# Kernel tuning notes

Hardware: AMD Instinct MI355X
Metric: run time of the kernel (lower is better)

Reference implementation:

```python
import jax, jax.numpy as jnp
import numpy as np

B, S, D = 64, 256, 768   # batch, max_seq_length, bert hidden
CAP = 8                  # semantic_cap_size (= num_capsules)
NT = 10                  # ntasks (= num_routes)
TASK = 5
NUM_ITER = 3


def squash(t, axis=-1):
    sq = jnp.sum(t * t, axis=axis, keepdims=True)
    return (sq / (1.0 + sq)) * t / jnp.sqrt(sq)


def setup_inputs() -> dict:
    key = jax.random.key(0)
    k0, k1, k2, k3 = jax.random.split(key, 4)
    x = jax.random.normal(k0, (B, S, D), dtype=jnp.float32)
    # per-task semantic projections: ntasks x Linear(768 -> CAP)
    fc1_w = jax.random.normal(k1, (NT, CAP, D), dtype=jnp.float32) * 0.02
    fc1_b = jnp.zeros((NT, CAP), dtype=jnp.float32)
    # route_weights: [num_capsules, num_routes, in_channel=S*CAP, class_dim=S]
    route_weights = jax.random.normal(k2, (CAP, NT, S * CAP, S), dtype=jnp.float32)
    # larger: Linear(CAP -> 768)
    larger_w = jax.random.normal(k3, (D, CAP), dtype=jnp.float32) * 0.02
    larger_b = jnp.zeros((D,), dtype=jnp.float32)
    return {"x": x, "task": TASK, "fc1_w": fc1_w, "fc1_b": fc1_b,
            "route_weights": route_weights, "larger_w": larger_w, "larger_b": larger_b}


def reference(x, task, fc1_w, fc1_b, route_weights, larger_w, larger_b):
    Bb, Ss, _ = x.shape
    nt, cap, _ = fc1_w.shape
    # --- semantic capsules: per-task Linear, cat over task dim, squash over tasks ---
    sem = jnp.einsum('bsd,ncd->bscn', x, fc1_w) + fc1_b.T[None, None]  # [B,S,CAP,NT]
    sem = sem.reshape(Bb, Ss * cap, nt)          # matches torch view(B,-1,1)+cat
    sem = squash(sem, axis=-1)
    u = jnp.transpose(sem, (0, 2, 1))            # [B, NT, S*CAP] (transpose(2,1))
    # --- tsv capsules: dynamic routing ---
    priors = jnp.einsum('brk,crkl->cbrl', u, route_weights)[:, :, :, None, :]  # [CAP,B,NT,1,S]
    tsv = jnp.tril(jnp.ones((nt, nt), dtype=x.dtype))
    tsv_t = tsv[task].reshape(1, 1, nt, 1, 1)
    mask = jnp.where(tsv[task] == 0, jnp.float32(-10000.0), jnp.float32(0.0)).reshape(1, 1, nt, 1, 1)
    logits = jnp.zeros_like(priors)
    vote = None
    for i in range(NUM_ITER):
        logits = logits * tsv_t + mask
        probs = jax.nn.softmax(logits, axis=2)                     # softmax over routes
        vote = jnp.sum(probs * priors, axis=2, keepdims=True)      # [CAP,B,1,1,S]
        out = squash(vote, axis=-1)
        if i != NUM_ITER - 1:
            logits = logits + jnp.sum(priors * out, axis=-1, keepdims=True)
    # torch .view on contiguous [CAP,B,1,1,S] -> (B, S, CAP): row-major reinterpret
    h = vote.reshape(-1).reshape(Bb, Ss, cap)
    return h @ larger_w.T + larger_b
```

## Files before the change

### kernel.cpp

```cpp
#include <hip/hip_runtime.h>
#include <hip/hip_bf16.h>

#define Bq 64
#define Sq 256
#define Dq 768
#define CAPq 8
#define NTq 10
#define SCq 2048

typedef short bf16x8 __attribute__((ext_vector_type(8)));
typedef float f32x4  __attribute__((ext_vector_type(4)));

static __device__ __forceinline__ short bfhi(float f) {
    return (short)(__float_as_uint(f) >> 16);
}
static __device__ __forceinline__ short bflo(float f) {
    float hi = __uint_as_float(__float_as_uint(f) & 0xFFFF0000u);
    return (short)(__float_as_uint(f - hi) >> 16);
}

__global__ __launch_bounds__(256) void k0_cvt(const float* __restrict__ w,
                                              short* __restrict__ hi,
                                              short* __restrict__ lo) {
    int i = blockIdx.x * 256 + threadIdx.x;
    if (i < NTq * CAPq * Dq) {
        int k8 = i / 640;
        int rem = i - k8 * 640;
        int o = rem >> 3, kf = rem & 7;
        float f = w[o * Dq + k8 * 8 + kf];
        hi[i] = bfhi(f);
        lo[i] = bflo(f);
    }
}

__device__ __forceinline__ void k1_comp(const float* xv, const short* pwh, const short* pwl,
                                        int ko80, f32x4* acc) {
    bf16x8 ah, al;
#pragma unroll
    for (int i = 0; i < 8; ++i) { ah[i] = bfhi(xv[i]); al[i] = bflo(xv[i]); }
#pragma unroll
    for (int f = 0; f < 5; ++f) {
        bf16x8 bh = *reinterpret_cast<const bf16x8*>(pwh + ko80 + f * 128);
        bf16x8 bl = *reinterpret_cast<const bf16x8*>(pwl + ko80 + f * 128);
        acc[f] = __builtin_amdgcn_mfma_f32_16x16x32_bf16(al, bh, acc[f], 0, 0, 0);
        acc[f] = __builtin_amdgcn_mfma_f32_16x16x32_bf16(ah, bl, acc[f], 0, 0, 0);
        acc[f] = __builtin_amdgcn_mfma_f32_16x16x32_bf16(ah, bh, acc[f], 0, 0, 0);
    }
}

__global__ __launch_bounds__(256) void k1_sem(const float* __restrict__ x,
                                              const short* __restrict__ fwh,
                                              const short* __restrict__ fwl,
                                              const float* __restrict__ fc1b,
                                              short* __restrict__ u_hi,
                                              short* __restrict__ u_lo) {
    __shared__ float redS[3][20][64];
    const int t = threadIdx.x;
    const int L = t & 63, w = t >> 6;
    const int colL = L & 15, kg = L >> 4;
    const int rowA = blockIdx.x * 16 + colL;

    f32x4 acc[5];
#pragma unroll
    for (int f = 0; f < 5; ++f) acc[f] = (f32x4){0.f, 0.f, 0.f, 0.f};

    const float* px = x + (size_t)rowA * Dq + w * 192 + kg * 8;
    const short* pwh = fwh + kg * 640 + colL * 8;
    const short* pwl = fwl + kg * 640 + colL * 8;

    float xv0[8], xv1[8];
    *reinterpret_cast<float4*>(&xv0[0]) = *reinterpret_cast<const float4*>(px);
    *reinterpret_cast<float4*>(&xv0[4]) = *reinterpret_cast<const float4*>(px + 4);

    for (int kc = 0; kc < 192; kc += 64) {
        {
            const float* p = px + kc + 32;
            *reinterpret_cast<float4*>(&xv1[0]) = *reinterpret_cast<const float4*>(p);
            *reinterpret_cast<float4*>(&xv1[4]) = *reinterpret_cast<const float4*>(p + 4);
        }
        __builtin_amdgcn_sched_barrier(0);
        k1_comp(xv0, pwh, pwl, (w * 192 + kc) * 80, acc);
        __builtin_amdgcn_sched_barrier(0);
        {
            int kn = (kc + 64 < 192) ? kc + 64 : 0;
            const float* p = px + kn;
            *reinterpret_cast<float4*>(&xv0[0]) = *reinterpret_cast<const float4*>(p);
            *reinterpret_cast<float4*>(&xv0[4]) = *reinterpret_cast<const float4*>(p + 4);
        }
        __builtin_amdgcn_sched_barrier(0);
        k1_comp(xv1, pwh, pwl, (w * 192 + kc + 32) * 80, acc);
        __builtin_amdgcn_sched_barrier(0);
    }

    if (w > 0) {
#pragma unroll
        for (int f = 0; f < 5; ++f)
#pragma unroll
            for (int g = 0; g < 4; ++g)
                redS[w - 1][f * 4 + g][L] = acc[f][g];
    }
    __syncthreads();
    if (w == 0) {
        float bias[5];
#pragma unroll
        for (int f = 0; f < 5; ++f) bias[f] = fc1b[f * 16 + colL];
        const int cc = colL & 7;
        const int npar = (colL >> 3) & 1;
#pragma unroll
        for (int reg = 0; reg < 4; ++reg) {
            const int row = blockIdx.x * 16 + kg * 4 + reg;
            const int b = row >> 8, s = row & 255;
            float v[5], sqp = 0.f;
#pragma unroll
            for (int f = 0; f < 5; ++f) {
                v[f] = acc[f][reg] + redS[0][f * 4 + reg][L] + redS[1][f * 4 + reg][L]
                     + redS[2][f * 4 + reg][L] + bias[f];
                sqp = fmaf(v[f], v[f], sqp);
            }
            float sq = sqp + __shfl_xor(sqp, 8, 64);
            float scale = (sq / (1.f + sq)) / sqrtf(sq);
#pragma unroll
            for (int f = 0; f < 5; ++f) {
                int n = 2 * f + npar;
                size_t off = (((size_t)n * 256 + s) * 64 + b) * 8 + cc;
                float val = v[f] * scale;
                u_hi[off] = bfhi(val);
                u_lo[off] = bflo(val);
            }
        }
    }
}

__device__ __forceinline__ void k2_comp(const float* bv, const short* puh, const short* pul,
                                        int ao, f32x4* acc) {
    bf16x8 bh, bl;
#pragma unroll
    for (int i = 0; i < 8; ++i) { bh[i] = bfhi(bv[i]); bl[i] = bflo(bv[i]); }
#pragma unroll
    for (int m = 0; m < 4; ++m) {
        bf16x8 ah = *reinterpret_cast<const bf16x8*>(puh + ao + m * 128);
        bf16x8 al = *reinterpret_cast<const bf16x8*>(pul + ao + m * 128);
        acc[m] = __builtin_amdgcn_mfma_f32_16x16x32_bf16(al, bh, acc[m], 0, 0, 0);
        acc[m] = __builtin_amdgcn_mfma_f32_16x16x32_bf16(ah, bl, acc[m], 0, 0, 0);
        acc[m] = __builtin_amdgcn_mfma_f32_16x16x32_bf16(ah, bh, acc[m], 0, 0, 0);
    }
}

__global__ __launch_bounds__(512) void k2_priors(const short* __restrict__ u_hi,
                                                 const short* __restrict__ u_lo,
                                                 const float* __restrict__ rw,
                                                 const int* __restrict__ task_p,
                                                 float* __restrict__ part) {
    const int r = blockIdx.y;
    if (r > *task_p) return;
    __shared__ float redS[3][2][16][64];
    const int t = threadIdx.x;
    const int L = t & 63, w = t >> 6;
    const int colL = L & 15, kg = L >> 4;
    const int lq = blockIdx.x & 7, ks = blockIdx.x >> 3;
    const int c = blockIdx.z;
    const int lh = w & 1, kh = w >> 1;
    const int l = lq * 32 + lh * 16 + colL;
    const int kw0 = ks * 1024 + kh * 256;
    const int s00 = kw0 >> 3;

    f32x4 acc[4];
#pragma unroll
    for (int m = 0; m < 4; ++m) acc[m] = (f32x4){0.f, 0.f, 0.f, 0.f};

    const float* pb = rw + ((size_t)(c * NTq + r) * SCq + kw0 + kg * 8) * Sq + l;
    const short* puh = u_hi + (((size_t)r * 256 + s00 + kg) * 64 + colL) * 8;
    const short* pul = u_lo + (((size_t)r * 256 + s00 + kg) * 64 + colL) * 8;

    float bv0[8], bv1[8];
#pragma unroll
    for (int i = 0; i < 8; ++i) bv0[i] = pb[(size_t)i * Sq];

    for (int kc = 0; kc < 256; kc += 64) {
        {
            const float* p = pb + (size_t)(kc + 32) * Sq;
#pragma unroll
            for (int i = 0; i < 8; ++i) bv1[i] = p[(size_t)i * Sq];
        }
        __builtin_amdgcn_sched_barrier(0);
        k2_comp(bv0, puh, pul, kc * 64, acc);
        __builtin_amdgcn_sched_barrier(0);
        {
            int kn = (kc + 64 < 256) ? kc + 64 : 0;
            const float* p = pb + (size_t)kn * Sq;
#pragma unroll
            for (int i = 0; i < 8; ++i) bv0[i] = p[(size_t)i * Sq];
        }
        __builtin_amdgcn_sched_barrier(0);
        k2_comp(bv1, puh, pul, (kc + 32) * 64, acc);
        __builtin_amdgcn_sched_barrier(0);
    }

    if (kh > 0) {
#pragma unroll
        for (int m = 0; m < 4; ++m)
#pragma unroll
            for (int g = 0; g < 4; ++g)
                redS[kh - 1][lh][m * 4 + g][L] = acc[m][g];
    }
    __syncthreads();
    if (kh == 0) {
#pragma unroll
        for (int m = 0; m < 4; ++m) {
#pragma unroll
            for (int g = 0; g < 4; ++g) {
                float v = acc[m][g] + redS[0][lh][m * 4 + g][L]
                        + redS[1][lh][m * 4 + g][L] + redS[2][lh][m * 4 + g][L];
                int b = m * 16 + kg * 4 + g;
                part[(size_t)ks * 1310720 + ((size_t)(c * Bq + b) * NTq + r) * Sq + l] = v;
            }
        }
    }
}

__global__ __launch_bounds__(256) void k3_route(const float* __restrict__ part,
                                                const int* __restrict__ task_p,
                                                float* __restrict__ vote_out) {
    const int t = threadIdx.x;
    const int lane = t & 63, w = t >> 6;
    const int wid = blockIdx.x * 4 + w;
    const int b = wid & 63, c = wid >> 6;
    const int task = *task_p;

    float pr[NTq][4];
    const float* p0 = part + ((size_t)(c * Bq + b) * NTq) * Sq + lane * 4;
#pragma unroll
    for (int r = 0; r < NTq; ++r) {
        f32x4 a = *reinterpret_cast<const f32x4*>(p0 + r * Sq);
        f32x4 d = *reinterpret_cast<const f32x4*>(p0 + 1310720 + r * Sq);
#pragma unroll
        for (int ii = 0; ii < 4; ++ii) pr[r][ii] = a[ii] + d[ii];
    }

    float logits[NTq];
#pragma unroll
    for (int r = 0; r < NTq; ++r) logits[r] = 0.f;
    float vote[4];

    for (int it = 0; it < 3; ++it) {
        float m = -1e30f;
#pragma unroll
        for (int r = 0; r < NTq; ++r) if (r <= task) m = fmaxf(m, logits[r]);
        float p[NTq]; float s = 0.f;
#pragma unroll
        for (int r = 0; r < NTq; ++r) {
            p[r] = (r <= task) ? expf(logits[r] - m) : 0.f;
            s += p[r];
        }
        float inv = 1.f / s;
#pragma unroll
        for (int ii = 0; ii < 4; ++ii) vote[ii] = 0.f;
#pragma unroll
        for (int r = 0; r < NTq; ++r) {
            float pw = p[r] * inv;
#pragma unroll
            for (int ii = 0; ii < 4; ++ii) vote[ii] = fmaf(pw, pr[r][ii], vote[ii]);
        }
        if (it == 2) break;

        float vals[11];
#pragma unroll
        for (int r = 0; r < NTq; ++r) {
            float d = 0.f;
#pragma unroll
            for (int ii = 0; ii < 4; ++ii) d = fmaf(pr[r][ii], vote[ii], d);
            vals[r] = d;
        }
        {
            float d = 0.f;
#pragma unroll
            for (int ii = 0; ii < 4; ++ii) d = fmaf(vote[ii], vote[ii], d);
            vals[10] = d;
        }
#pragma unroll
        for (int o = 32; o > 0; o >>= 1) {
#pragma unroll
            for (int v = 0; v < 11; ++v) vals[v] += __shfl_xor(vals[v], o, 64);
        }
        float sq = vals[10];
        float scale = (sq / (1.f + sq)) / sqrtf(sq);
#pragma unroll
        for (int r = 0; r < NTq; ++r)
            if (r <= task) logits[r] += scale * vals[r];
    }

    f32x4 vo;
#pragma unroll
    for (int ii = 0; ii < 4; ++ii) vo[ii] = vote[ii];
    *reinterpret_cast<f32x4*>(vote_out + (size_t)(c * Bq + b) * Sq + lane * 4) = vo;
}

__global__ __launch_bounds__(256) void k4_out(const float* __restrict__ vote,
                                              const float* __restrict__ lw,
                                              const float* __restrict__ lb,
                                              float* __restrict__ out) {
    __shared__ float hS[8][8];
    const int t = threadIdx.x;
    if (t < 64) {
        int rr = t >> 3, cc = t & 7;
        size_t row = (size_t)blockIdx.x * 8 + rr;
        size_t flat = row * 8 + cc;
        int c = (int)(flat >> 14);
        int rem = (int)(flat & 16383);
        int bb = rem >> 8;
        int l = rem & 255;
        hS[rr][cc] = vote[(size_t)c*16384 + bb*256 + l];
    }
    float lwr[3][8];
    float lbr[3];
#pragma unroll
    for (int dd = 0; dd < 3; ++dd) {
        int d = t + dd*256;
        float4 a = *reinterpret_cast<const float4*>(&lw[(size_t)d*8]);
        float4 b2 = *reinterpret_cast<const float4*>(&lw[(size_t)d*8 + 4]);
        lwr[dd][0]=a.x; lwr[dd][1]=a.y; lwr[dd][2]=a.z; lwr[dd][3]=a.w;
        lwr[dd][4]=b2.x; lwr[dd][5]=b2.y; lwr[dd][6]=b2.z; lwr[dd][7]=b2.w;
        lbr[dd] = lb[d];
    }
    __syncthreads();
#pragma unroll
    for (int rr = 0; rr < 8; ++rr) {
        size_t row = (size_t)blockIdx.x * 8 + rr;
#pragma unroll
        for (int dd = 0; dd < 3; ++dd) {
            float acc = lbr[dd];
#pragma unroll
            for (int c = 0; c < 8; ++c) acc = fmaf(hS[rr][c], lwr[dd][c], acc);
            out[row*Dq + t + dd*256] = acc;
        }
    }
}

extern "C" void kernel_launch(void* const* d_in, const int* in_sizes, int n_in,
                              void* d_out, int out_size, void* d_ws, size_t ws_size,
                              hipStream_t stream) {
    const float* x    = (const float*)d_in[0];
    const int*   task = (const int*)d_in[1];
    const float* fc1w = (const float*)d_in[2];
    const float* fc1b = (const float*)d_in[3];
    const float* rw   = (const float*)d_in[4];
    const float* lw   = (const float*)d_in[5];
    const float* lb   = (const float*)d_in[6];
    float* out = (float*)d_out;

    short* u_hi = (short*)d_ws;
    short* u_lo = u_hi + 1310720;
    float* part = (float*)((char*)d_ws + 5242880);
    float* vote = part + 2621440;
    short* fwh  = (short*)((char*)d_ws + 16252928);
    short* fwl  = fwh + 61440;

    k0_cvt<<<240, 256, 0, stream>>>(fc1w, fwh, fwl);
    k1_sem<<<1024, 256, 0, stream>>>(x, fwh, fwl, fc1b, u_hi, u_lo);
    dim3 g2(16, NTq, CAPq);
    k2_priors<<<g2, 512, 0, stream>>>(u_hi, u_lo, rw, task, part);
    k3_route<<<128, 256, 0, stream>>>(part, task, vote);
    k4_out<<<2048, 256, 0, stream>>>(vote, lw, lb, out);
}
```

Before: 78.06 us.

## Widen k2 priors tiles to paired columns and fuse routing with output projection

The priors kernel now has each thread handle two adjacent output columns. It loads route weights as float2 and runs two accumulator sets, which halves the thread count per block and reuses each u fragment across both columns. The routing kernel is fused with the final Linear(8->768): the vote values are redistributed by shuffles inside the wave, and the output rows are written directly. This removes the vote round-trip through global memory and one kernel launch. In exchange, register pressure in k2 rises (launch bounds 256,3), and the fused kernel does every block's FMAs for 12 output chunks per lane.

```diff
diff --git a/kernel.cpp b/kernel.cpp
--- a/kernel.cpp
+++ b/kernel.cpp
@@ -131,68 +131,76 @@
     }
 }
 
-__device__ __forceinline__ void k2_comp(const float* bv, const short* puh, const short* pul,
-                                        int ao, f32x4* acc) {
-    bf16x8 bh, bl;
-#pragma unroll
-    for (int i = 0; i < 8; ++i) { bh[i] = bfhi(bv[i]); bl[i] = bflo(bv[i]); }
+__device__ __forceinline__ void k2_comp2(const float2* bv, const short* puh, const short* pul,
+                                         int ao, f32x4* accE, f32x4* accO) {
+    bf16x8 bhE, blE, bhO, blO;
+#pragma unroll
+    for (int i = 0; i < 8; ++i) {
+        bhE[i] = bfhi(bv[i].x); blE[i] = bflo(bv[i].x);
+        bhO[i] = bfhi(bv[i].y); blO[i] = bflo(bv[i].y);
+    }
 #pragma unroll
     for (int m = 0; m < 4; ++m) {
         bf16x8 ah = *reinterpret_cast<const bf16x8*>(puh + ao + m * 128);
         bf16x8 al = *reinterpret_cast<const bf16x8*>(pul + ao + m * 128);
-        acc[m] = __builtin_amdgcn_mfma_f32_16x16x32_bf16(al, bh, acc[m], 0, 0, 0);
-        acc[m] = __builtin_amdgcn_mfma_f32_16x16x32_bf16(ah, bl, acc[m], 0, 0, 0);
-        acc[m] = __builtin_amdgcn_mfma_f32_16x16x32_bf16(ah, bh, acc[m], 0, 0, 0);
-    }
-}
-
-__global__ __launch_bounds__(512) void k2_priors(const short* __restrict__ u_hi,
-                                                 const short* __restrict__ u_lo,
-                                                 const float* __restrict__ rw,
-                                                 const int* __restrict__ task_p,
-                                                 float* __restrict__ part) {
+        accE[m] = __builtin_amdgcn_mfma_f32_16x16x32_bf16(al, bhE, accE[m], 0, 0, 0);
+        accE[m] = __builtin_amdgcn_mfma_f32_16x16x32_bf16(ah, blE, accE[m], 0, 0, 0);
+        accE[m] = __builtin_amdgcn_mfma_f32_16x16x32_bf16(ah, bhE, accE[m], 0, 0, 0);
+        accO[m] = __builtin_amdgcn_mfma_f32_16x16x32_bf16(al, bhO, accO[m], 0, 0, 0);
+        accO[m] = __builtin_amdgcn_mfma_f32_16x16x32_bf16(ah, blO, accO[m], 0, 0, 0);
+        accO[m] = __builtin_amdgcn_mfma_f32_16x16x32_bf16(ah, bhO, accO[m], 0, 0, 0);
+    }
+}
+
+__global__ __launch_bounds__(256, 3) void k2_priors(const short* __restrict__ u_hi,
+                                                    const short* __restrict__ u_lo,
+                                                    const float* __restrict__ rw,
+                                                    const int* __restrict__ task_p,
+                                                    float* __restrict__ part) {
     const int r = blockIdx.y;
     if (r > *task_p) return;
     __shared__ float redS[3][2][16][64];
     const int t = threadIdx.x;
-    const int L = t & 63, w = t >> 6;
+    const int L = t & 63, kh = t >> 6;
     const int colL = L & 15, kg = L >> 4;
     const int lq = blockIdx.x & 7, ks = blockIdx.x >> 3;
     const int c = blockIdx.z;
-    const int lh = w & 1, kh = w >> 1;
-    const int l = lq * 32 + lh * 16 + colL;
+    const int le = lq * 32 + 2 * colL;
     const int kw0 = ks * 1024 + kh * 256;
     const int s00 = kw0 >> 3;
 
-    f32x4 acc[4];
-#pragma unroll
-    for (int m = 0; m < 4; ++m) acc[m] = (f32x4){0.f, 0.f, 0.f, 0.f};
-
-    const float* pb = rw + ((size_t)(c * NTq + r) * SCq + kw0 + kg * 8) * Sq + l;
+    f32x4 accE[4], accO[4];
+#pragma unroll
+    for (int m = 0; m < 4; ++m) {
+        accE[m] = (f32x4){0.f, 0.f, 0.f, 0.f};
+        accO[m] = (f32x4){0.f, 0.f, 0.f, 0.f};
+    }
+
+    const float* pb = rw + ((size_t)(c * NTq + r) * SCq + kw0 + kg * 8) * Sq + le;
     const short* puh = u_hi + (((size_t)r * 256 + s00 + kg) * 64 + colL) * 8;
     const short* pul = u_lo + (((size_t)r * 256 + s00 + kg) * 64 + colL) * 8;
 
-    float bv0[8], bv1[8];
-#pragma unroll
-    for (int i = 0; i < 8; ++i) bv0[i] = pb[(size_t)i * Sq];
+    float2 bv0[8], bv1[8];
+#pragma unroll
+    for (int i = 0; i < 8; ++i) bv0[i] = *reinterpret_cast<const float2*>(pb + (size_t)i * Sq);
 
     for (int kc = 0; kc < 256; kc += 64) {
         {
             const float* p = pb + (size_t)(kc + 32) * Sq;
 #pragma unroll
-            for (int i = 0; i < 8; ++i) bv1[i] = p[(size_t)i * Sq];
-        }
-        __builtin_amdgcn_sched_barrier(0);
-        k2_comp(bv0, puh, pul, kc * 64, acc);
+            for (int i = 0; i < 8; ++i) bv1[i] = *reinterpret_cast<const float2*>(p + (size_t)i * Sq);
+        }
+        __builtin_amdgcn_sched_barrier(0);
+        k2_comp2(bv0, puh, pul, kc * 64, accE, accO);
         __builtin_amdgcn_sched_barrier(0);
         {
             int kn = (kc + 64 < 256) ? kc + 64 : 0;
             const float* p = pb + (size_t)kn * Sq;
 #pragma unroll
-            for (int i = 0; i < 8; ++i) bv0[i] = p[(size_t)i * Sq];
-        }
-        __builtin_amdgcn_sched_barrier(0);
-        k2_comp(bv1, puh, pul, (kc + 32) * 64, acc);
+            for (int i = 0; i < 8; ++i) bv0[i] = *reinterpret_cast<const float2*>(p + (size_t)i * Sq);
+        }
+        __builtin_amdgcn_sched_barrier(0);
+        k2_comp2(bv1, puh, pul, (kc + 32) * 64, accE, accO);
         __builtin_amdgcn_sched_barrier(0);
     }
 
@@ -200,8 +208,10 @@
 #pragma unroll
         for (int m = 0; m < 4; ++m)
 #pragma unroll
-            for (int g = 0; g < 4; ++g)
-                redS[kh - 1][lh][m * 4 + g][L] = acc[m][g];
+            for (int g = 0; g < 4; ++g) {
+                redS[kh - 1][0][m * 4 + g][L] = accE[m][g];
+                redS[kh - 1][1][m * 4 + g][L] = accO[m][g];
+            }
     }
     __syncthreads();
     if (kh == 0) {
@@ -209,22 +219,27 @@
         for (int m = 0; m < 4; ++m) {
 #pragma unroll
             for (int g = 0; g < 4; ++g) {
-                float v = acc[m][g] + redS[0][lh][m * 4 + g][L]
-                        + redS[1][lh][m * 4 + g][L] + redS[2][lh][m * 4 + g][L];
-                int b = m * 16 + kg * 4 + g;
-                part[(size_t)ks * 1310720 + ((size_t)(c * Bq + b) * NTq + r) * Sq + l] = v;
+                float vE = accE[m][g] + redS[0][0][m * 4 + g][L]
+                         + redS[1][0][m * 4 + g][L] + redS[2][0][m * 4 + g][L];
+                float vO = accO[m][g] + redS[0][1][m * 4 + g][L]
+                         + redS[1][1][m * 4 + g][L] + redS[2][1][m * 4 + g][L];
+                int bb = m * 16 + kg * 4 + g;
+                size_t idx = (size_t)ks * 1310720 + ((size_t)(c * Bq + bb) * NTq + r) * Sq + le;
+                float2 vv; vv.x = vE; vv.y = vO;
+                *reinterpret_cast<float2*>(part + idx) = vv;
             }
         }
     }
 }
 
-__global__ __launch_bounds__(256) void k3_route(const float* __restrict__ part,
-                                                const int* __restrict__ task_p,
-                                                float* __restrict__ vote_out) {
+__global__ __launch_bounds__(256) void k34_route_out(const float* __restrict__ part,
+                                                     const int* __restrict__ task_p,
+                                                     const float* __restrict__ lw,
+                                                     const float* __restrict__ lb,
+                                                     float* __restrict__ out) {
     const int t = threadIdx.x;
     const int lane = t & 63, w = t >> 6;
-    const int wid = blockIdx.x * 4 + w;
-    const int b = wid & 63, c = wid >> 6;
+    const int b = blockIdx.x & 63, c = blockIdx.x >> 6;
     const int task = *task_p;
 
     float pr[NTq][4];
@@ -289,49 +304,34 @@
             if (r <= task) logits[r] += scale * vals[r];
     }
 
-    f32x4 vo;
-#pragma unroll
-    for (int ii = 0; ii < 4; ++ii) vo[ii] = vote[ii];
-    *reinterpret_cast<f32x4*>(vote_out + (size_t)(c * Bq + b) * Sq + lane * 4) = vo;
-}
-
-__global__ __launch_bounds__(256) void k4_out(const float* __restrict__ vote,
-                                              const float* __restrict__ lw,
-                                              const float* __restrict__ lb,
-                                              float* __restrict__ out) {
-    __shared__ float hS[8][8];
-    const int t = threadIdx.x;
-    if (t < 64) {
-        int rr = t >> 3, cc = t & 7;
-        size_t row = (size_t)blockIdx.x * 8 + rr;
-        size_t flat = row * 8 + cc;
-        int c = (int)(flat >> 14);
-        int rem = (int)(flat & 16383);
-        int bb = rem >> 8;
-        int l = rem & 255;
-        hS[rr][cc] = vote[(size_t)c*16384 + bb*256 + l];
-    }
-    float lwr[3][8];
-    float lbr[3];
-#pragma unroll
-    for (int dd = 0; dd < 3; ++dd) {
-        int d = t + dd*256;
-        float4 a = *reinterpret_cast<const float4*>(&lw[(size_t)d*8]);
-        float4 b2 = *reinterpret_cast<const float4*>(&lw[(size_t)d*8 + 4]);
-        lwr[dd][0]=a.x; lwr[dd][1]=a.y; lwr[dd][2]=a.z; lwr[dd][3]=a.w;
-        lwr[dd][4]=b2.x; lwr[dd][5]=b2.y; lwr[dd][6]=b2.z; lwr[dd][7]=b2.w;
-        lbr[dd] = lb[d];
-    }
-    __syncthreads();
-#pragma unroll
-    for (int rr = 0; rr < 8; ++rr) {
-        size_t row = (size_t)blockIdx.x * 8 + rr;
-#pragma unroll
-        for (int dd = 0; dd < 3; ++dd) {
-            float acc = lbr[dd];
-#pragma unroll
-            for (int c = 0; c < 8; ++c) acc = fmaf(hS[rr][c], lwr[dd][c], acc);
-            out[row*Dq + t + dd*256] = acc;
+    float v[8][8];
+#pragma unroll
+    for (int j = 0; j < 8; ++j) {
+        int s0 = w * 16 + 2 * j;
+#pragma unroll
+        for (int ii = 0; ii < 4; ++ii) v[j][ii]     = __shfl(vote[ii], s0, 64);
+#pragma unroll
+        for (int ii = 0; ii < 4; ++ii) v[j][4 + ii] = __shfl(vote[ii], s0 + 1, 64);
+    }
+    const int rbase = c * 2048 + b * 32 + w * 8;
+#pragma unroll
+    for (int dd = 0; dd < 12; ++dd) {
+        int d = lane + dd * 64;
+        float4 wa = *reinterpret_cast<const float4*>(lw + (size_t)d * 8);
+        float4 wb = *reinterpret_cast<const float4*>(lw + (size_t)d * 8 + 4);
+        float lbv = lb[d];
+#pragma unroll
+        for (int j = 0; j < 8; ++j) {
+            float acc = lbv;
+            acc = fmaf(v[j][0], wa.x, acc);
+            acc = fmaf(v[j][1], wa.y, acc);
+            acc = fmaf(v[j][2], wa.z, acc);
+            acc = fmaf(v[j][3], wa.w, acc);
+            acc = fmaf(v[j][4], wb.x, acc);
+            acc = fmaf(v[j][5], wb.y, acc);
+            acc = fmaf(v[j][6], wb.z, acc);
+            acc = fmaf(v[j][7], wb.w, acc);
+            out[(size_t)(rbase + j) * Dq + d] = acc;
         }
     }
 }
@@ -351,14 +351,12 @@
     short* u_hi = (short*)d_ws;
     short* u_lo = u_hi + 1310720;
     float* part = (float*)((char*)d_ws + 5242880);
-    float* vote = part + 2621440;
     short* fwh  = (short*)((char*)d_ws + 16252928);
     short* fwl  = fwh + 61440;
 
     k0_cvt<<<240, 256, 0, stream>>>(fc1w, fwh, fwl);
     k1_sem<<<1024, 256, 0, stream>>>(x, fwh, fwl, fc1b, u_hi, u_lo);
     dim3 g2(16, NTq, CAPq);
-    k2_priors<<<g2, 512, 0, stream>>>(u_hi, u_lo, rw, task, part);
-    k3_route<<<128, 256, 0, stream>>>(part, task, vote);
-    k4_out<<<2048, 256, 0, stream>>>(vote, lw, lb, out);
-}
+    k2_priors<<<g2, 256, 0, stream>>>(u_hi, u_lo, rw, task, part);
+    k34_route_out<<<512, 256, 0, stream>>>(part, task, lw, lb, out);
+}
```

Result: no change. 77.86 us (-0.3%).
